# Optimization experiments

Hardware: AMD Instinct MI355X
Metric: run time of the kernel (lower is better)

The kernel has to match this reference:

```python
import jax, jax.numpy as jnp
import numpy as np
import math

B, L, D, H = 8, 2048, 1024, 1024


def setup_inputs() -> dict:
    key = jax.random.key(0)
    ks = jax.random.split(key, 6)
    scale = 1.0 / math.sqrt(D)
    return {
        "input_q": jax.random.normal(ks[0], (B, L, D), dtype=jnp.float32),
        "input_k": jax.random.normal(ks[1], (B, L, D), dtype=jnp.float32),
        "k_mask": jax.random.uniform(ks[2], (B, L), dtype=jnp.float32),
        "Wq": jax.random.normal(ks[3], (D, H), dtype=jnp.float32) * scale,
        "bq": jnp.zeros((H,), dtype=jnp.float32),
        "Wk": jax.random.normal(ks[4], (D, H), dtype=jnp.float32) * scale,
        "bk": jnp.zeros((H,), dtype=jnp.float32),
    }


def reference(input_q, input_k, k_mask, Wq, bq, Wk, bk):
    # Linear projections: (b, l, d) @ (d, h) -> (b, l, h)
    q = input_q @ Wq + bq
    k = input_k @ Wk + bk
    # Faithful to original: mask values become 0.0 or -1e9, then an
    # outer product bmm((b,l,1),(b,1,l)) builds the (b,l,l) additive mask.
    m = jnp.where(k_mask > 0.5, 0.0, -1000000000.0)  # (b, l)
    add_mask = m[:, :, None] * m[:, None, :]          # (b, l, l) outer product
    # Scaled dot-product scores
    attn = jnp.einsum("bqh,bkh->bqk", q, k) / math.sqrt(H)
    attn = jax.nn.softmax(attn + add_mask, axis=-1)
    # Weighted sum over the ORIGINAL input_k (not projected k), as in source
    out = jnp.einsum("bqk,bkd->bqd", attn, input_k)
    return out
```

## Files before the change

### kernel.cpp

```cpp
#include <hip/hip_runtime.h>

#define BATCH 8
#define SEQ   2048
#define DIM   1024

typedef __attribute__((ext_vector_type(8)))  short short8;
typedef __attribute__((ext_vector_type(4)))  short short4v;
typedef __attribute__((ext_vector_type(4)))  float floatx4;
typedef __attribute__((ext_vector_type(16))) float floatx16;

__device__ __forceinline__ unsigned short f32_to_bf16(float f) {
    union { float f; unsigned int u; } x; x.f = f;
    unsigned int r = x.u + 0x7fffu + ((x.u >> 16) & 1u);
    return (unsigned short)(r >> 16);
}

__device__ __forceinline__ float bf16_to_f32(unsigned short h) {
    union { unsigned int u; float f; } x; x.u = ((unsigned int)h) << 16;
    return x.f;
}

__device__ __forceinline__ void async_load16(const void* g, void* l) {
    __builtin_amdgcn_global_load_lds(
        (const __attribute__((address_space(1))) void*)g,
        (__attribute__((address_space(3))) void*)l, 16, 0, 0);
}

__global__ __launch_bounds__(256) void build_idx(
    const float* __restrict__ mask, int* __restrict__ idx,
    int* __restrict__ cnt, int* __restrict__ padcnt)
{
    const int b = blockIdx.x;
    const int t = threadIdx.x;
    const float* mb = mask + b * SEQ;
    int flags[8]; int c = 0;
#pragma unroll
    for (int j = 0; j < 8; ++j) {
        flags[j] = (mb[t * 8 + j] > 0.5f) ? 1 : 0;
        c += flags[j];
    }
    int sc = c;
    for (int o = 1; o < 64; o <<= 1) {
        int v = __shfl_up(sc, o);
        if ((t & 63) >= o) sc += v;
    }
    __shared__ int wtot[4];
    const int lane = t & 63, wave = t >> 6;
    if (lane == 63) wtot[wave] = sc;
    __syncthreads();
    int woff = 0;
    for (int w = 0; w < wave; ++w) woff += wtot[w];
    int p = woff + sc - c;
#pragma unroll
    for (int j = 0; j < 8; ++j)
        if (flags[j]) idx[b * SEQ + (p++)] = t * 8 + j;
    __syncthreads();
    const int total = wtot[0] + wtot[1] + wtot[2] + wtot[3];
    if (t == 0) { cnt[b] = total; padcnt[b] = (total + 127) & ~127; }
    for (int q = total + t; q < SEQ; q += 256) idx[b * SEQ + q] = 0;
}

__global__ __launch_bounds__(256) void gather_cvt_q(
    const float* __restrict__ xq, const int* __restrict__ idx,
    const int* __restrict__ padcnt, unsigned short* __restrict__ qc)
{
    const int b = blockIdx.y;
    const int rc = blockIdx.x;
    if (rc >= padcnt[b]) return;
    const int src = idx[b * SEQ + rc];
    const float* s = xq + ((long)b * SEQ + src) * DIM + threadIdx.x * 4;
    unsigned short* d = qc + ((long)b * SEQ + rc) * DIM + threadIdx.x * 4;
    floatx4 v = *(const floatx4*)s;
    short4v w;
#pragma unroll
    for (int j = 0; j < 4; ++j) w[j] = (short)f32_to_bf16(v[j]);
    *(short4v*)d = w;
}

__global__ __launch_bounds__(256) void prep_kv(
    const float* __restrict__ xk, const float* __restrict__ mask,
    unsigned short* __restrict__ kbf, unsigned short* __restrict__ Vt,
    float* __restrict__ mavg)
{
    __shared__ float tile[32][33];
    __shared__ float msk[32];
    __shared__ float csum[8][32];
    const int b  = blockIdx.z;
    const int c0 = blockIdx.x * 32;
    const int r0 = blockIdx.y * 32;
    const int tx = threadIdx.x & 31, ty = threadIdx.x >> 5;
    const float* xb = xk + (long)b * SEQ * DIM;
    unsigned short* kb = kbf + (long)b * SEQ * DIM;
    unsigned short* vb = Vt + (long)b * DIM * SEQ;

    if (threadIdx.x < 32) msk[threadIdx.x] = mask[b * SEQ + r0 + threadIdx.x];

    float v[4];
#pragma unroll
    for (int i = 0; i < 4; ++i) {
        const int r = ty + i * 8;
        v[i] = xb[(long)(r0 + r) * DIM + c0 + tx];
        tile[r][tx] = v[i];
        kb[(long)(r0 + r) * DIM + c0 + tx] = f32_to_bf16(v[i]);
    }
    __syncthreads();

    float s = 0.f;
#pragma unroll
    for (int i = 0; i < 4; ++i) {
        const int r = ty + i * 8;
        s += (msk[r] <= 0.5f) ? v[i] : 0.f;
    }
    csum[ty][tx] = s;

#pragma unroll
    for (int i = 0; i < 4; ++i) {
        const int c = ty + i * 8;
        vb[(long)(c0 + c) * SEQ + r0 + tx] = f32_to_bf16(tile[tx][c]);
    }
    __syncthreads();
    if (ty == 0) {
        float t = 0.f;
#pragma unroll
        for (int j = 0; j < 8; ++j) t += csum[j][tx];
        atomicAdd(&mavg[b * DIM + c0 + tx], t);
    }
}

__global__ __launch_bounds__(256) void cvt_bf16(
    const float* __restrict__ src, unsigned short* __restrict__ dst)
{
    const long i = ((long)blockIdx.x * 256 + threadIdx.x) * 8;
    floatx4 v0 = *(const floatx4*)(src + i);
    floatx4 v1 = *(const floatx4*)(src + i + 4);
    short8 w;
#pragma unroll
    for (int j = 0; j < 4; ++j) w[j]     = (short)f32_to_bf16(v0[j]);
#pragma unroll
    for (int j = 0; j < 4; ++j) w[4 + j] = (short)f32_to_bf16(v1[j]);
    *(short8*)(dst + i) = w;
}

__global__ __launch_bounds__(256) void proj_bias(
    const float* __restrict__ bq, const float* __restrict__ Wk, float* __restrict__ g0)
{
    const int n = blockIdx.x;
    const int t = threadIdx.x;
    float s = 0.f;
    for (int h = t; h < DIM; h += 256) s += bq[h] * Wk[(long)n * DIM + h];
    for (int o = 32; o; o >>= 1) s += __shfl_xor(s, o);
    __shared__ float r[4];
    if ((t & 63) == 0) r[t >> 6] = s;
    __syncthreads();
    if (t == 0) g0[n] = r[0] + r[1] + r[2] + r[3];
}

template<bool C_BF16, bool BIAS, bool LIMIT, bool SCATTER, int FLAT>
__global__ __launch_bounds__(256) void gemm_bt(
    const unsigned short* __restrict__ A, const unsigned short* __restrict__ Bt,
    void* __restrict__ Cp, const float* __restrict__ bias,
    int N, int K, long sA, long sB, long sC, float scale,
    const int* __restrict__ mlim, const int* __restrict__ cntp,
    const int* __restrict__ idx, int sh)
{
    int bx, by, bz;
    if (FLAT == 0) {
        bx = blockIdx.x; by = blockIdx.y; bz = blockIdx.z;
    } else {
        const int id = blockIdx.x;
        bz = id & 7;
        const int rem = id >> 3;
        const int m = (1 << sh) - 1;
        if (FLAT == 1) { bx = rem & m; by = rem >> sh; }
        else           { by = rem & m; bx = rem >> sh; }
    }
    const int row0 = bx * 128;
    if (LIMIT && row0 >= mlim[bz]) return;

    __shared__ unsigned short As[128 * 64];
    __shared__ unsigned short Bs[128 * 64];

    const int tid  = threadIdx.x;
    const int lane = tid & 63;
    const int wave = tid >> 6;
    const int wm   = wave >> 1;
    const int wn   = wave & 1;
    const int l31  = lane & 31;
    const int half = lane >> 5;
    const int x7   = lane & 7;
    const int col0 = by * 128;
    const long zA = (long)bz * sA;
    const long zB = (long)bz * sB;
    const long zC = (long)bz * sC;

    const int sr = lane >> 3;
    const int sq = ((lane & 7) ^ sr) * 8;

    const unsigned short* Abase = A  + zA + (long)row0 * K;
    const unsigned short* Bbase = Bt + zB + (long)col0 * K;
    const unsigned short* aptr[4];
    const unsigned short* bptr[4];
#pragma unroll
    for (int c = 0; c < 4; ++c) {
        const int r = (wave * 4 + c) * 8 + sr;
        aptr[c] = Abase + (long)r * K + sq;
        bptr[c] = Bbase + (long)r * K + sq;
    }

    floatx16 acc[2][2];
#pragma unroll
    for (int a = 0; a < 2; ++a)
#pragma unroll
        for (int b = 0; b < 2; ++b)
#pragma unroll
            for (int r = 0; r < 16; ++r) acc[a][b][r] = 0.f;

    const int raf[2] = { (wm * 64 +  0 + l31) * 64, (wm * 64 + 32 + l31) * 64 };
    const int rbf[2] = { (wn * 64 +  0 + l31) * 64, (wn * 64 + 32 + l31) * 64 };

    for (int kt = 0; kt < K; kt += 64) {
#pragma unroll
        for (int c = 0; c < 4; ++c) {
            const int chunk = wave * 4 + c;
            async_load16(aptr[c] + kt, As + chunk * 512);
            async_load16(bptr[c] + kt, Bs + chunk * 512);
        }
        __syncthreads();

#pragma unroll
        for (int ks = 0; ks < 4; ++ks) {
            const int sw = ((ks * 2 + half) ^ x7) << 3;
            short8 af[2], bf[2];
#pragma unroll
            for (int t = 0; t < 2; ++t) {
                af[t] = *(const short8*)(As + raf[t] + sw);
                bf[t] = *(const short8*)(Bs + rbf[t] + sw);
            }
#pragma unroll
            for (int tm = 0; tm < 2; ++tm)
#pragma unroll
                for (int tn = 0; tn < 2; ++tn)
                    acc[tm][tn] = __builtin_amdgcn_mfma_f32_32x32x16_bf16(
                        af[tm], bf[tn], acc[tm][tn], 0, 0, 0);
        }
        __syncthreads();
    }

    const int climit = SCATTER ? cntp[bz] : 0;
    const int* ridx  = SCATTER ? (idx + bz * SEQ) : (const int*)nullptr;
#pragma unroll
    for (int tn = 0; tn < 2; ++tn) {
        const int ccol = col0 + wn * 64 + tn * 32 + l31;
        float bv = 0.f;
        if (BIAS) bv = bias[ccol];
#pragma unroll
        for (int tm = 0; tm < 2; ++tm) {
            const int rbase = row0 + wm * 64 + tm * 32 + 4 * half;
#pragma unroll
            for (int r = 0; r < 16; ++r) {
                const int crow = rbase + (r & 3) + 8 * (r >> 2);
                float v = acc[tm][tn][r] * scale + bv;
                long orow = crow;
                if (SCATTER) {
                    if (crow >= climit) continue;
                    orow = ridx[crow];
                }
                const long ci = zC + orow * (long)N + ccol;
                if (C_BF16) ((unsigned short*)Cp)[ci] = f32_to_bf16(v);
                else        ((float*)Cp)[ci] = v;
            }
        }
    }
}

__global__ __launch_bounds__(256) void softmax_rows(
    unsigned short* __restrict__ S, const int* __restrict__ padcnt)
{
    const int b = blockIdx.x >> 11, rc = blockIdx.x & 2047;
    if (rc >= padcnt[b]) return;
    const long base = (long)blockIdx.x * SEQ + threadIdx.x * 8;
    const int lane = threadIdx.x & 63, wave = threadIdx.x >> 6;
    __shared__ float rbuf[8];

    short8 v = *(const short8*)(S + base);
    float x[8];
#pragma unroll
    for (int j = 0; j < 8; ++j) x[j] = bf16_to_f32((unsigned short)v[j]);

    float m = x[0];
#pragma unroll
    for (int j = 1; j < 8; ++j) m = fmaxf(m, x[j]);
    for (int o = 32; o; o >>= 1) m = fmaxf(m, __shfl_xor(m, o));
    if (lane == 0) rbuf[wave] = m;
    __syncthreads();
    m = fmaxf(fmaxf(rbuf[0], rbuf[1]), fmaxf(rbuf[2], rbuf[3]));

    float e[8], s = 0.f;
#pragma unroll
    for (int j = 0; j < 8; ++j) { e[j] = __expf(x[j] - m); s += e[j]; }
    for (int o = 32; o; o >>= 1) s += __shfl_xor(s, o);
    if (lane == 0) rbuf[4 + wave] = s;
    __syncthreads();
    s = rbuf[4] + rbuf[5] + rbuf[6] + rbuf[7];
    const float inv = 1.0f / s;

    short8 o8;
#pragma unroll
    for (int j = 0; j < 8; ++j) o8[j] = (short)f32_to_bf16(e[j] * inv);
    *(short8*)(S + base) = o8;
}

__global__ __launch_bounds__(256) void overwrite_masked(
    float* __restrict__ out, const float* __restrict__ mask,
    const float* __restrict__ mavg, const int* __restrict__ cnt)
{
    const int bid = blockIdx.x;
    const int b = bid >> 11;
    if (mask[bid] > 0.5f) return;
    const float inv = 1.0f / (float)(SEQ - cnt[b]);
    const long obase = (long)bid * DIM;
    const float* mv = mavg + b * DIM;
    for (int d = threadIdx.x; d < DIM; d += 256)
        out[obase + d] = mv[d] * inv;
}

extern "C" void kernel_launch(void* const* d_in, const int* in_sizes, int n_in,
                              void* d_out, int out_size, void* d_ws, size_t ws_size,
                              hipStream_t stream) {
    (void)in_sizes; (void)n_in; (void)out_size;
    const float* input_q = (const float*)d_in[0];
    const float* input_k = (const float*)d_in[1];
    const float* k_mask  = (const float*)d_in[2];
    const float* Wq      = (const float*)d_in[3];
    const float* bq      = (const float*)d_in[4];
    const float* Wk      = (const float*)d_in[5];
    const float* bk      = (const float*)d_in[6];
    (void)bk;
    float* out = (float*)d_out;

    char* ws = (char*)d_ws;
    unsigned short* qc   = (unsigned short*)(ws);
    unsigned short* S    = (unsigned short*)(ws);
    unsigned short* qpp  = (unsigned short*)(ws + 67108864);
    unsigned short* Wqb  = (unsigned short*)(ws + 67108864);
    unsigned short* Wkb  = (unsigned short*)(ws + 69206016);
    unsigned short* kbf  = (unsigned short*)(ws + 100663296);
    unsigned short* Vt   = (unsigned short*)(ws + 134217728);
    unsigned short* Gt   = (unsigned short*)(ws + 167772160);
    float*          g0   = (float*)(ws + 169869312);
    float*          mavg = (float*)(ws + 169873408);
    int*            idx  = (int*)(ws + 169906176);
    int*            cnts = (int*)(ws + 169971712);
    int*            pcnt = (int*)(ws + 169971744);
    if (ws_size < 169971776) return;

    hipMemsetAsync(mavg, 0, BATCH * DIM * sizeof(float), stream);

    build_idx<<<BATCH, 256, 0, stream>>>(k_mask, idx, cnts, pcnt);
    gather_cvt_q<<<dim3(SEQ, BATCH), 256, 0, stream>>>(input_q, idx, pcnt, qc);
    prep_kv<<<dim3(DIM / 32, SEQ / 32, BATCH), 256, 0, stream>>>(input_k, k_mask, kbf, Vt, mavg);
    cvt_bf16<<<512, 256, 0, stream>>>(Wq, Wqb);
    cvt_bf16<<<512, 256, 0, stream>>>(Wk, Wkb);
    proj_bias<<<DIM, 256, 0, stream>>>(bq, Wk, g0);

    gemm_bt<true, false, false, false, 0><<<dim3(8, 8, 1), 256, 0, stream>>>(
        Wkb, Wqb, Gt, nullptr, DIM, DIM, 0, 0, 0, 1.0f, nullptr, nullptr, nullptr, 0);

    gemm_bt<true, true, true, false, 2><<<8 * 16 * 8, 256, 0, stream>>>(
        qc, Gt, qpp, g0, DIM, DIM,
        (long)SEQ * DIM, 0, (long)SEQ * DIM, 1.0f, pcnt, nullptr, nullptr, 3);

    gemm_bt<true, false, true, false, 1><<<8 * 16 * 16, 256, 0, stream>>>(
        qpp, kbf, S, nullptr, SEQ, DIM,
        (long)SEQ * DIM, (long)SEQ * DIM, (long)SEQ * SEQ, 0.03125f, pcnt, nullptr, nullptr, 4);

    softmax_rows<<<BATCH * SEQ, 256, 0, stream>>>(S, pcnt);

    gemm_bt<false, false, true, true, 2><<<8 * 16 * 8, 256, 0, stream>>>(
        S, Vt, out, nullptr, DIM, SEQ,
        (long)SEQ * SEQ, (long)DIM * SEQ, (long)SEQ * DIM, 1.0f, pcnt, cnts, idx, 3);

    overwrite_masked<<<BATCH * SEQ, 256, 0, stream>>>(out, k_mask, mavg, cnts);
}
```

Baseline: 365.5 us.

## Merge weight conversions, cut GEMM address registers, request four blocks per CU

The two bf16 weight-conversion launches become a single launch that picks its source by block index, saving one kernel launch. The GEMM kernel now keeps one row pointer per operand plus a stride instead of eight precomputed pointers, and defers the C-stride computation until the epilogue, which lowers register pressure. __launch_bounds__(256, 4) asks the compiler for enough occupancy to fit four blocks per CU, which could cause spills if registers are tight.

```diff
diff --git a/kernel.cpp b/kernel.cpp
--- a/kernel.cpp
+++ b/kernel.cpp
@@ -127,10 +127,14 @@
     }
 }
 
-__global__ __launch_bounds__(256) void cvt_bf16(
-    const float* __restrict__ src, unsigned short* __restrict__ dst)
-{
-    const long i = ((long)blockIdx.x * 256 + threadIdx.x) * 8;
+__global__ __launch_bounds__(256) void cvt_bf16_2(
+    const float* __restrict__ s0, unsigned short* __restrict__ d0,
+    const float* __restrict__ s1, unsigned short* __restrict__ d1)
+{
+    const int hi = blockIdx.x >> 9;
+    const float* src = hi ? s1 : s0;
+    unsigned short* dst = hi ? d1 : d0;
+    const long i = ((long)(blockIdx.x & 511) * 256 + threadIdx.x) * 8;
     floatx4 v0 = *(const floatx4*)(src + i);
     floatx4 v1 = *(const floatx4*)(src + i + 4);
     short8 w;
@@ -156,7 +160,7 @@
 }
 
 template<bool C_BF16, bool BIAS, bool LIMIT, bool SCATTER, int FLAT>
-__global__ __launch_bounds__(256) void gemm_bt(
+__global__ __launch_bounds__(256, 4) void gemm_bt(
     const unsigned short* __restrict__ A, const unsigned short* __restrict__ Bt,
     void* __restrict__ Cp, const float* __restrict__ bias,
     int N, int K, long sA, long sB, long sC, float scale,
@@ -189,23 +193,15 @@
     const int half = lane >> 5;
     const int x7   = lane & 7;
     const int col0 = by * 128;
-    const long zA = (long)bz * sA;
-    const long zB = (long)bz * sB;
-    const long zC = (long)bz * sC;
 
     const int sr = lane >> 3;
     const int sq = ((lane & 7) ^ sr) * 8;
 
-    const unsigned short* Abase = A  + zA + (long)row0 * K;
-    const unsigned short* Bbase = Bt + zB + (long)col0 * K;
-    const unsigned short* aptr[4];
-    const unsigned short* bptr[4];
-#pragma unroll
-    for (int c = 0; c < 4; ++c) {
-        const int r = (wave * 4 + c) * 8 + sr;
-        aptr[c] = Abase + (long)r * K + sq;
-        bptr[c] = Bbase + (long)r * K + sq;
-    }
+    const long K8 = (long)K * 8;
+    const unsigned short* aRow =
+        A + (long)bz * sA + (long)row0 * K + (long)(wave * 32 + sr) * K + sq;
+    const unsigned short* bRow =
+        Bt + (long)bz * sB + (long)col0 * K + (long)(wave * 32 + sr) * K + sq;
 
     floatx16 acc[2][2];
 #pragma unroll
@@ -222,8 +218,8 @@
 #pragma unroll
         for (int c = 0; c < 4; ++c) {
             const int chunk = wave * 4 + c;
-            async_load16(aptr[c] + kt, As + chunk * 512);
-            async_load16(bptr[c] + kt, Bs + chunk * 512);
+            async_load16(aRow + kt + c * K8, As + chunk * 512);
+            async_load16(bRow + kt + c * K8, Bs + chunk * 512);
         }
         __syncthreads();
 
@@ -246,6 +242,7 @@
         __syncthreads();
     }
 
+    const long zC = (long)bz * sC;
     const int climit = SCATTER ? cntp[bz] : 0;
     const int* ridx  = SCATTER ? (idx + bz * SEQ) : (const int*)nullptr;
 #pragma unroll
@@ -359,8 +356,7 @@
     build_idx<<<BATCH, 256, 0, stream>>>(k_mask, idx, cnts, pcnt);
     gather_cvt_q<<<dim3(SEQ, BATCH), 256, 0, stream>>>(input_q, idx, pcnt, qc);
     prep_kv<<<dim3(DIM / 32, SEQ / 32, BATCH), 256, 0, stream>>>(input_k, k_mask, kbf, Vt, mavg);
-    cvt_bf16<<<512, 256, 0, stream>>>(Wq, Wqb);
-    cvt_bf16<<<512, 256, 0, stream>>>(Wk, Wkb);
+    cvt_bf16_2<<<1024, 256, 0, stream>>>(Wq, Wqb, Wk, Wkb);
     proj_bias<<<DIM, 256, 0, stream>>>(bq, Wk, g0);
 
     gemm_bt<true, false, false, false, 0><<<dim3(8, 8, 1), 256, 0, stream>>>(
```

After: 371.0 us. No clear change (+1.5%).
